# Optimization experiments

Hardware: AMD Instinct MI355X
Metric: run time of the kernel (lower is better)

The kernel has to match this reference:

```python
import jax, jax.numpy as jnp
import numpy as np
from jax import lax

# Dimensions
B, CIN, COUT = 8, 3, 3
NF = 128          # num_features
K = 9             # DISCO kernel_shape (number of filter basis functions)
HLAT, WLON = 181, 360   # in_shape == out_shape (1-degree equiangular sphere grid)
KH, KW = 5, 5     # compact lat/lon support of each DISCO basis function


def setup_inputs() -> dict:
    key = jax.random.key(0)
    ks = jax.random.split(key, 10)
    s = lambda fan: 1.0 / np.sqrt(fan)
    return {
        "x": jax.random.normal(ks[0], (B, CIN, HLAT, WLON), jnp.float32),
        # DISCO conv: latitude-dependent basis filters, quadrature weights, channel mix
        "psi": jax.random.normal(ks[1], (K, HLAT, KH, KW), jnp.float32) * s(KH * KW),
        "quad": jnp.abs(jax.random.normal(ks[2], (HLAT,), jnp.float32)) * (1.0 / HLAT)
                + jnp.sin(jnp.pi * (jnp.arange(HLAT) + 0.5) / HLAT) * (1.0 / HLAT),
        "w1": jax.random.normal(ks[3], (NF, CIN, K), jnp.float32) * s(CIN * K),
        "b1": jnp.zeros((NF,), jnp.float32),
        # standard conv2d stages
        "w2": jax.random.normal(ks[4], (NF // 2, NF, 5, 5), jnp.float32) * s(NF * 25),
        "b2": jnp.zeros((NF // 2,), jnp.float32),
        "w3": jax.random.normal(ks[5], (COUT, NF // 2, 5, 5), jnp.float32) * s(NF // 2 * 25),
        "b3": jnp.zeros((COUT,), jnp.float32),
    }


def _disco_conv_s2(x, psi, quad, w, b):
    """Discrete-continuous spherical conv: latitude-dependent gather + weighted sum.
    x: [B,C,H,W]; psi: [K,H,KH,KW]; quad: [H]; w: [O,C,K]; b: [O] -> [B,O,H,W]"""
    H, W = x.shape[-2], x.shape[-1]
    rh, rw = KH // 2, KW // 2
    xw = x * quad[None, None, :, None]                       # quadrature-weighted input
    # neighborhood indices: clipped in latitude, circular in longitude
    hi = jnp.clip(jnp.arange(H)[:, None] + jnp.arange(KH)[None, :] - rh, 0, H - 1)  # [H,KH]
    wi = (jnp.arange(W)[:, None] + jnp.arange(KW)[None, :] - rw) % W                # [W,KW]
    g = xw[:, :, hi, :]                                      # [B,C,H,KH,W]
    patches = g[:, :, :, :, wi]                              # [B,C,H,KH,W,KW]
    # project onto latitude-dependent filter basis, then mix channels per basis
    z = jnp.einsum('khij,bchiwj->bckhw', psi, patches)       # [B,C,K,H,W]
    return jnp.einsum('ock,bckhw->bohw', w, z) + b[None, :, None, None]


def _conv2d(x, w, b, pad):
    y = lax.conv_general_dilated(x, w, (1, 1), [(pad, pad), (pad, pad)],
                                 dimension_numbers=('NCHW', 'OIHW', 'NCHW'))
    return y + b[None, :, None, None]


def reference(x, psi, quad, w1, b1, w2, b2, w3, b3):
    h = jax.nn.relu(_disco_conv_s2(x, psi, quad, w1, b1))
    h = jax.nn.relu(_conv2d(h, w2, b2, 2))
    return _conv2d(h, w3, b3, 2)
```

## Files before the change

### kernel.cpp

```cpp
#include <hip/hip_runtime.h>
#include <hip/hip_bf16.h>

#define HLAT 181
#define WLON 360
#define HW (HLAT * WLON)
#define HPAD 188
#define WPAD 368
#define PCHH ((size_t)HPAD * WPAD * 8)
#define W2P 372
#define PLANE2 ((size_t)HPAD * W2P * 64)
#define ZROW ((size_t)12 * 4 * 32 * 16)

typedef __attribute__((ext_vector_type(4)))  short short4v;
typedef __attribute__((ext_vector_type(8)))  short short8v;
typedef __attribute__((ext_vector_type(4)))  float f32x4;
typedef __attribute__((ext_vector_type(16))) float f32x16;

static __device__ __forceinline__ ushort bf16_hi_bits(float f) {
  union { float f; unsigned u; } c; c.f = f;
  unsigned u = c.u;
  unsigned rounded = u + 0x7FFF + ((u >> 16) & 1);
  return (ushort)(rounded >> 16);
}
static __device__ __forceinline__ float bf16_to_f(ushort b) {
  union { unsigned u; float f; } c; c.u = ((unsigned)b) << 16;
  return c.f;
}

__global__ __launch_bounds__(256) void k_tw(const float* __restrict__ w2,
                                            const float* __restrict__ w3,
                                            const float* __restrict__ w1,
                                            const float* __restrict__ b1,
                                            ushort* __restrict__ w2f,
                                            ushort* __restrict__ w1f,
                                            ushort* __restrict__ w3f) {
  int idx = blockIdx.x * 256 + threadIdx.x;
  if (idx < 51200) {
    int l   = idx & 63;
    int p   = (idx >> 6) & 1;
    int m   = (idx >> 7) & 1;
    int ch  = (idx >> 8) & 7;
    int tap = idx >> 11;
    int oc  = m * 32 + (l & 31);
    int ci0 = ch * 16 + (l >> 5) * 8;
#pragma unroll
    for (int j = 0; j < 8; ++j) {
      float f = w2[(oc * 128 + ci0 + j) * 25 + tap];
      ushort hi = bf16_hi_bits(f);
      w2f[(size_t)idx * 8 + j] = (p == 0) ? hi : bf16_hi_bits(f - bf16_to_f(hi));
    }
  }
  if (idx < 1024) {
    int l = idx & 63;
    int e = idx >> 6;
    int p  = e & 1;
    int kc = (e >> 1) & 1;
    int m  = e >> 2;
    int oc = m * 32 + (l & 31);
    int k0 = kc * 16 + (l >> 5) * 8;
#pragma unroll
    for (int j = 0; j < 8; ++j) {
      int k = k0 + j;
      float f = (k < 27) ? w1[oc * 27 + k] : (k == 27 ? b1[oc] : 0.f);
      ushort hi = bf16_hi_bits(f);
      w1f[(size_t)idx * 8 + j] = (p == 0) ? hi : bf16_hi_bits(f - bf16_to_f(hi));
    }
  }
  if (idx < 6400) {
    int l   = idx & 63;
    int p   = (idx >> 6) & 1;
    int kc  = (idx >> 7) & 1;
    int tap = idx >> 8;
    int oc  = l & 15;
    int ci0 = kc * 32 + (l >> 4) * 8;
#pragma unroll
    for (int j = 0; j < 8; ++j) {
      float f = (oc < 3) ? w3[(oc * 64 + ci0 + j) * 25 + tap] : 0.f;
      ushort hi = bf16_hi_bits(f);
      w3f[(size_t)idx * 8 + j] = (p == 0) ? hi : bf16_hi_bits(f - bf16_to_f(hi));
    }
  }
}

__global__ __launch_bounds__(256) void k_zring(ushort* __restrict__ h1s) {
  const int i = blockIdx.x * 256 + threadIdx.x;
  if (i >= 4024) return;
  int row, col;
  if (i < 736)       { row = i / 368;              col = i % 368; }
  else if (i < 2576) { int p = i - 736;  row = 183 + p / 368; col = p % 368; }
  else if (i < 2938) { int p = i - 2576; row = 2 + p % 181;   col = p / 181; }
  else               { int p = i - 2938; row = 2 + p % 181;   col = 362 + p / 181; }
  short8v z = {0, 0, 0, 0, 0, 0, 0, 0};
  *(short8v*)(h1s + (size_t)blockIdx.y * PCHH + ((size_t)row * 368 + col) * 8) = z;
}

__global__ __launch_bounds__(256) void k_zring2(ushort* __restrict__ h2p) {
  const int i = blockIdx.x * 256 + threadIdx.x;
  if (i >= 4776) return;
  int row, col;
  if (i < 744)       { row = i / W2P;             col = i % W2P; }
  else if (i < 2604) { int p = i - 744;  row = 183 + p / W2P; col = p % W2P; }
  else               { int p = i - 2604; row = 2 + p % 181;
                       int cI = p / 181; col = (cI < 2) ? cI : 360 + cI; }
  short8v z = {0, 0, 0, 0, 0, 0, 0, 0};
  short8v* d = (short8v*)(h2p + (size_t)blockIdx.y * PLANE2 + ((size_t)row * W2P + col) * 64);
#pragma unroll
  for (int k = 0; k < 8; ++k) d[k] = z;
}

__global__ __launch_bounds__(384, 2) void k_z(const float* __restrict__ x,
    const float* __restrict__ psi, const float* __restrict__ quad,
    ushort* __restrict__ zbuf, int b0) {
  const int h = blockIdx.x;
  const int bi = blockIdx.y;
  const int b = b0 + bi;
  const int tid = threadIdx.x;
  float z[28];
#pragma unroll
  for (int q = 0; q < 28; ++q) z[q] = 0.f;
  if (tid < 360) {
#pragma unroll 1
    for (int i = 0; i < 5; ++i) {
      int hi = h + i - 2;
      hi = hi < 0 ? 0 : (hi >= HLAT ? HLAT - 1 : hi);
      const float qv = quad[hi];
      float pv[45];
#pragma unroll
      for (int kk = 0; kk < 9; ++kk)
#pragma unroll
        for (int j = 0; j < 5; ++j)
          pv[kk * 5 + j] = psi[((size_t)(kk * HLAT + h)) * 25 + i * 5 + j];
#pragma unroll
      for (int c = 0; c < 3; ++c) {
        const float* row = x + ((size_t)(b * 3 + c) * HLAT + hi) * WLON;
        float v[5];
#pragma unroll
        for (int j = 0; j < 5; ++j) {
          int wj = tid + j - 2;
          wj = wj < 0 ? wj + WLON : (wj >= WLON ? wj - WLON : wj);
          v[j] = row[wj] * qv;
        }
#pragma unroll
        for (int kk = 0; kk < 9; ++kk) {
          float a = 0.f;
#pragma unroll
          for (int j = 0; j < 5; ++j) a += pv[kk * 5 + j] * v[j];
          z[c * 9 + kk] += a;
        }
      }
    }
    z[27] = 1.0f;
  }
  ushort hiv[32], lov[32];
#pragma unroll
  for (int q = 0; q < 28; ++q) {
    const ushort hb = bf16_hi_bits(z[q]);
    hiv[q] = hb;
    lov[q] = bf16_hi_bits(z[q] - bf16_to_f(hb));
  }
#pragma unroll
  for (int q = 28; q < 32; ++q) { hiv[q] = 0; lov[q] = 0; }

  ushort* tb = zbuf + (size_t)(bi * HLAT + h) * ZROW +
               (size_t)(tid >> 5) * 2048 + (size_t)(tid & 31) * 16;
#pragma unroll
  for (int pk = 0; pk < 4; ++pk) {
    const ushort* src = (pk < 2 ? hiv : lov) + (pk & 1) * 16;
    union { ushort u[8]; short8v v8; } a0, a1;
#pragma unroll
    for (int j = 0; j < 8; ++j) { a0.u[j] = src[j]; a1.u[j] = src[8 + j]; }
    *(short8v*)(tb + (size_t)pk * 512 + 0) = a0.v8;
    *(short8v*)(tb + (size_t)pk * 512 + 8) = a1.v8;
  }
}

__global__ __launch_bounds__(256, 2) void k_mv(const ushort* __restrict__ zbuf,
    const ushort* __restrict__ w1f, ushort* __restrict__ h1s) {
  __shared__ ushort st[4][16][32][16];
  const int h = blockIdx.x;
  const int bi = blockIdx.y;
  const int tid = threadIdx.x;
  const int wv = tid >> 6;
  const int l = tid & 63;
  const int l31 = l & 31;
  const int q = l >> 5;
  const short8v* wf1 = (const short8v*)w1f;
  short8v A[4][2][2];
#pragma unroll
  for (int m = 0; m < 4; ++m)
#pragma unroll
    for (int kc = 0; kc < 2; ++kc)
#pragma unroll
      for (int p = 0; p < 2; ++p)
        A[m][kc][p] = wf1[(size_t)(((m * 2 + kc) * 2 + p) * 64 + l)];

  ushort* base = h1s + (size_t)bi * 32 * PCHH;
  const ushort* zrow = zbuf + (size_t)(bi * HLAT + h) * ZROW;
#pragma unroll
  for (int nn = 0; nn < 3; ++nn) {
    const int n = wv * 3 + nn;
    const ushort* zn = zrow + (size_t)n * 2048 + l31 * 16 + q * 8;
    const short8v bh0 = *(const short8v*)(zn + 0);
    const short8v bh1 = *(const short8v*)(zn + 512);
    const short8v bl0 = *(const short8v*)(zn + 1024);
    const short8v bl1 = *(const short8v*)(zn + 1536);
#pragma unroll
    for (int m = 0; m < 4; ++m) {
      f32x16 acc;
#pragma unroll
      for (int e = 0; e < 16; ++e) acc[e] = 0.f;
      acc = __builtin_amdgcn_mfma_f32_32x32x16_bf16(A[m][0][0], bh0, acc, 0, 0, 0);
      acc = __builtin_amdgcn_mfma_f32_32x32x16_bf16(A[m][0][1], bh0, acc, 0, 0, 0);
      acc = __builtin_amdgcn_mfma_f32_32x32x16_bf16(A[m][0][0], bl0, acc, 0, 0, 0);
      acc = __builtin_amdgcn_mfma_f32_32x32x16_bf16(A[m][1][0], bh1, acc, 0, 0, 0);
      acc = __builtin_amdgcn_mfma_f32_32x32x16_bf16(A[m][1][1], bh1, acc, 0, 0, 0);
      acc = __builtin_amdgcn_mfma_f32_32x32x16_bf16(A[m][1][0], bl1, acc, 0, 0, 0);
#pragma unroll
      for (int r = 0; r < 4; ++r) {
        const int rb = 8 * r + 4 * q;
        const int p2h = m * 2 + (rb >> 4);
        const int ci0 = rb & 15;
        short4v h4, l4;
#pragma unroll
        for (int j = 0; j < 4; ++j) {
          const float v = fmaxf(acc[r * 4 + j], 0.f);
          const ushort hb = bf16_hi_bits(v);
          h4[j] = (short)hb;
          l4[j] = (short)bf16_hi_bits(v - bf16_to_f(hb));
        }
        *(short4v*)&st[wv][p2h][l31][ci0] = h4;
        *(short4v*)&st[wv][8 + p2h][l31][ci0] = l4;
      }
    }
    const int pxr = n * 32 + (l >> 1);
    if (pxr < 360) {
      const size_t po = ((size_t)(h + 2) * WPAD + (pxr + 2)) * 8;
#pragma unroll
      for (int p2 = 0; p2 < 16; ++p2) {
        const short8v v = *(const short8v*)&st[wv][p2][l >> 1][(l & 1) * 8];
        *(short8v*)(base + (size_t)(p2 * 2 + (l & 1)) * PCHH + po) = v;
      }
    }
  }
}

__global__ __launch_bounds__(256, 2) void k_conv2(const ushort* __restrict__ h1s,
    const ushort* __restrict__ w2f, const float* __restrict__ b2,
    ushort* __restrict__ h2p) {
  __shared__ ushort act[2][15360];
  const int x0 = blockIdx.x * 32;
  const int y0 = blockIdx.y * 8;
  const int bi = blockIdx.z;
  const int tid = threadIdx.x;
  const int wv = tid >> 6;
  const int m  = wv >> 1;
  const int wr = wv & 1;
  const int l = tid & 63;
  const int l31 = l & 31;
  const int q = l >> 5;

  f32x16 acc[4];
#pragma unroll
  for (int r = 0; r < 4; ++r)
#pragma unroll
    for (int e = 0; e < 16; ++e) acc[r][e] = 0.f;

  const short8v* wf = (const short8v*)w2f;
  const ushort* pbase = h1s + (size_t)bi * 32 * PCHH;

  unsigned goff[8];
#pragma unroll
  for (int s = 0; s < 8; ++s) {
    const int idx = (wv * 8 + s) * 64 + l;
    const int reg = idx / 480;
    const int rem = idx - reg * 480;
    const int t = rem / 40;
    const int c = rem - t * 40;
    const int part = reg >> 1, qq = reg & 1;
    goff[s] = (unsigned)((part * 16 + qq) * PCHH) +
              (unsigned)(((y0 + t) * WPAD + (x0 + c)) * 8);
  }

  auto stage = [&](int buf, int ch) {
    const size_t choff = (size_t)ch * 2 * PCHH;
#pragma unroll
    for (int s = 0; s < 8; ++s) {
      if (wv * 8 + s < 30) {
        const ushort* g = pbase + choff + goff[s];
        ushort* d = &act[buf][(wv * 8 + s) * 512];
        __builtin_amdgcn_global_load_lds(
            (const __attribute__((address_space(1))) unsigned int*)g,
            (__attribute__((address_space(3))) unsigned int*)d, 16, 0, 0);
      }
    }
  };

  stage(0, 0);
  asm volatile("s_waitcnt vmcnt(0)" ::: "memory");
  __syncthreads();

#pragma unroll 1
  for (int ch = 0; ch < 8; ++ch) {
    const int cur = ch & 1;
    if (ch < 7) stage(cur ^ 1, ch + 1);
#pragma unroll 1
    for (int dj = 0; dj < 5; ++dj) {
      short8v aw[5][2];
#pragma unroll
      for (int di = 0; di < 5; ++di) {
        const size_t e0 = (size_t)(((di * 5 + dj) * 8 + ch) * 4 + m * 2) * 64 + l;
        aw[di][0] = wf[e0];
        aw[di][1] = wf[e0 + 64];
      }
      const unsigned rbase = q * 3840 + (l31 + dj) * 8;
      __builtin_amdgcn_s_setprio(1);
#pragma unroll
      for (int rr = 0; rr < 8; ++rr) {
        const int t = wr * 4 + rr;
        const short8v bh = *(const short8v*)&act[cur][rbase + t * 320];
        const short8v bl = *(const short8v*)&act[cur][7680 + rbase + t * 320];
#pragma unroll
        for (int di = 0; di < 5; ++di) {
          const int r = rr - di;
          if (r < 0 || r > 3) continue;
          acc[r] = __builtin_amdgcn_mfma_f32_32x32x16_bf16(aw[di][0], bh, acc[r], 0, 0, 0);
          acc[r] = __builtin_amdgcn_mfma_f32_32x32x16_bf16(aw[di][1], bh, acc[r], 0, 0, 0);
          acc[r] = __builtin_amdgcn_mfma_f32_32x32x16_bf16(aw[di][0], bl, acc[r], 0, 0, 0);
        }
      }
      __builtin_amdgcn_s_setprio(0);
    }
    asm volatile("s_waitcnt vmcnt(0)" ::: "memory");
    __syncthreads();
  }

  const int xg = x0 + l31;
  ushort* hp = h2p + (size_t)bi * 2 * PLANE2;
  if (xg < WLON) {
#pragma unroll
    for (int r = 0; r < 4; ++r) {
      const int y = y0 + wr * 4 + r;
      if (y >= HLAT) continue;
      const size_t po = ((size_t)(y + 2) * W2P + (xg + 2)) * 64;
#pragma unroll
      for (int run = 0; run < 4; ++run) {
        const int oc0 = m * 32 + 8 * run + 4 * q;
        short4v h4, l4;
#pragma unroll
        for (int j = 0; j < 4; ++j) {
          const float v = fmaxf(acc[r][run * 4 + j] + b2[oc0 + j], 0.f);
          const ushort hb = bf16_hi_bits(v);
          h4[j] = (short)hb;
          l4[j] = (short)bf16_hi_bits(v - bf16_to_f(hb));
        }
        *(short4v*)(hp + po + oc0) = h4;
        *(short4v*)(hp + PLANE2 + po + oc0) = l4;
      }
    }
  }
}

__global__ __launch_bounds__(256, 2) void k_conv3(const ushort* __restrict__ h2p,
    const ushort* __restrict__ w3f, const float* __restrict__ b3,
    float* __restrict__ out, int b0) {
  __shared__ ushort act[2][12][20][72];
  const int x0 = blockIdx.x * 16;
  const int y0 = blockIdx.y * 8;
  const int bi = blockIdx.z;
  const int tid = threadIdx.x;
  const int wv = tid >> 6;
  const int l = tid & 63;

  {
    const ushort* pb = h2p + (size_t)bi * 2 * PLANE2;
    float4 v[6][3];
#pragma unroll
    for (int pr = 0; pr < 6; ++pr) {
      const int pair = wv * 6 + pr;
      const int part = pair / 12;
      const int row = pair % 12;
      const ushort* src = pb + (size_t)part * PLANE2 +
                          ((size_t)(y0 + row) * W2P + x0) * 64;
      v[pr][0] = *(const float4*)((const char*)src + l * 16);
      v[pr][1] = *(const float4*)((const char*)src + 1024 + l * 16);
      if (l < 32) v[pr][2] = *(const float4*)((const char*)src + 2048 + l * 16);
    }
#pragma unroll
    for (int pr = 0; pr < 6; ++pr) {
      const int pair = wv * 6 + pr;
      const int part = pair / 12;
      const int row = pair % 12;
#pragma unroll
      for (int k2 = 0; k2 < 3; ++k2) {
        if (k2 == 2 && l >= 32) continue;
        const int B = k2 * 1024 + l * 16;
        const int col = B >> 7;
        const int ci = (B & 127) >> 1;
        *(short8v*)&act[part][row][col][ci] = *(short8v*)&v[pr][k2];
      }
    }
  }
  __syncthreads();

  f32x4 acc[2];
#pragma unroll
  for (int r = 0; r < 2; ++r)
#pragma unroll
    for (int e = 0; e < 4; ++e) acc[r][e] = 0.f;

  const short8v* wf3 = (const short8v*)w3f;
  const int c16 = l & 15;
  const int koff0 = ((l >> 4) & 3) * 8;

#pragma unroll 1
  for (int kc = 0; kc < 2; ++kc) {
#pragma unroll 1
    for (int dj = 0; dj < 5; ++dj) {
      short8v A[5][2];
#pragma unroll
      for (int di = 0; di < 5; ++di) {
        const size_t e0 = (size_t)(((di * 5 + dj) * 2 + kc) * 2) * 64 + l;
        A[di][0] = wf3[e0];
        A[di][1] = wf3[e0 + 64];
      }
      const int c = c16 + dj;
      const int koff = kc * 32 + koff0;
      __builtin_amdgcn_s_setprio(1);
#pragma unroll
      for (int tt = 0; tt < 6; ++tt) {
        const int t = wv * 2 + tt;
        const short8v bh = *(const short8v*)&act[0][t][c][koff];
        const short8v bl = *(const short8v*)&act[1][t][c][koff];
#pragma unroll
        for (int di = 0; di < 5; ++di) {
          const int r = tt - di;
          if (r < 0 || r > 1) continue;
          acc[r] = __builtin_amdgcn_mfma_f32_16x16x32_bf16(A[di][0], bh, acc[r], 0, 0, 0);
          acc[r] = __builtin_amdgcn_mfma_f32_16x16x32_bf16(A[di][1], bh, acc[r], 0, 0, 0);
          acc[r] = __builtin_amdgcn_mfma_f32_16x16x32_bf16(A[di][0], bl, acc[r], 0, 0, 0);
        }
      }
      __builtin_amdgcn_s_setprio(0);
    }
  }

  const int px = x0 + c16;
  const int b = b0 + bi;
  if ((l >> 4) == 0 && px < WLON) {
    const float bb[3] = {b3[0], b3[1], b3[2]};
#pragma unroll
    for (int r = 0; r < 2; ++r) {
      const int y = y0 + wv * 2 + r;
      if (y >= HLAT) continue;
#pragma unroll
      for (int j = 0; j < 3; ++j)
        out[((size_t)(b * 3 + j) * HLAT + y) * WLON + px] = acc[r][j] + bb[j];
    }
  }
}

extern "C" void kernel_launch(void* const* d_in, const int* in_sizes, int n_in,
                              void* d_out, int out_size, void* d_ws, size_t ws_size,
                              hipStream_t stream) {
  const float* x    = (const float*)d_in[0];
  const float* psi  = (const float*)d_in[1];
  const float* quad = (const float*)d_in[2];
  const float* w1   = (const float*)d_in[3];
  const float* b1   = (const float*)d_in[4];
  const float* w2   = (const float*)d_in[5];
  const float* b2   = (const float*)d_in[6];
  const float* w3   = (const float*)d_in[7];
  const float* b3   = (const float*)d_in[8];
  float* out = (float*)d_out;
  float* ws  = (float*)d_ws;

  ushort* w2f = (ushort*)ws;
  ushort* w1f = (ushort*)(ws + 204800);
  ushort* w3f = (ushort*)(ws + 208896);
  const size_t HEAD = 234496;

  size_t wsf = ws_size / 4;
  const size_t h1s_f = PCHH * 16;
  const size_t h2p_f = PLANE2;
  const size_t per_b = h1s_f + h2p_f;
  int bc = 8;
  while (bc > 1 && HEAD + (size_t)bc * per_b > wsf) bc >>= 1;

  ushort* h1s = (ushort*)(ws + HEAD);
  ushort* h2p = (ushort*)(ws + HEAD + (size_t)bc * h1s_f);
  ushort* zbuf = h2p;

  k_tw<<<dim3(200), dim3(256), 0, stream>>>(w2, w3, w1, b1, w2f, w1f, w3f);
  k_zring<<<dim3(16, bc * 32), dim3(256), 0, stream>>>(h1s);

  for (int b0 = 0; b0 < 8; b0 += bc) {
    int cur = 8 - b0 < bc ? 8 - b0 : bc;
    k_z<<<dim3(HLAT, cur), dim3(384), 0, stream>>>(x, psi, quad, zbuf, b0);
    k_mv<<<dim3(HLAT, cur), dim3(256), 0, stream>>>(zbuf, w1f, h1s);
    k_zring2<<<dim3(19, cur * 2), dim3(256), 0, stream>>>(h2p);
    k_conv2<<<dim3(12, 23, cur), dim3(256), 0, stream>>>(h1s, w2f, b2, h2p);
    k_conv3<<<dim3(23, 23, cur), dim3(256), 0, stream>>>(h2p, w3f, b3, out, b0);
  }
}
```

Before: 763.1 us.

## Split conv2 into 8-wave blocks staging hi and lo activation parts separately

Doubles the conv2 block from 4 to 8 waves, with each wave computing 2 output rows instead of 4. This halves the accumulator registers and raises the occupancy target. Activation staging is split into separate hi and lo bf16 parts held in two half-size LDS buffers. The hi part runs the two weight-split MFMAs and the lo part runs one MFMA. This halves shared memory per block and frees registers, but it adds a barrier per part and exposes load latency, since the next channel's hi part is loaded only after the lo buffer is ready. Each wave also reloads the weight fragments for every row group.

After: 878.7 us. 1.15x slower.

```diff
diff --git a/kernel.cpp b/kernel.cpp
--- a/kernel.cpp
+++ b/kernel.cpp
@@ -244,50 +244,49 @@
   }
 }
 
-__global__ __launch_bounds__(256, 2) void k_conv2(const ushort* __restrict__ h1s,
+__global__ __launch_bounds__(512, 4) void k_conv2(const ushort* __restrict__ h1s,
     const ushort* __restrict__ w2f, const float* __restrict__ b2,
     ushort* __restrict__ h2p) {
-  __shared__ ushort act[2][15360];
+  __shared__ ushort act[2][7680];
   const int x0 = blockIdx.x * 32;
   const int y0 = blockIdx.y * 8;
   const int bi = blockIdx.z;
   const int tid = threadIdx.x;
   const int wv = tid >> 6;
-  const int m  = wv >> 1;
-  const int wr = wv & 1;
+  const int m  = wv >> 2;
+  const int wr = wv & 3;
   const int l = tid & 63;
   const int l31 = l & 31;
   const int q = l >> 5;
 
-  f32x16 acc[4];
-#pragma unroll
-  for (int r = 0; r < 4; ++r)
+  f32x16 acc[2];
+#pragma unroll
+  for (int r = 0; r < 2; ++r)
 #pragma unroll
     for (int e = 0; e < 16; ++e) acc[r][e] = 0.f;
 
   const short8v* wf = (const short8v*)w2f;
   const ushort* pbase = h1s + (size_t)bi * 32 * PCHH;
 
-  unsigned goff[8];
-#pragma unroll
-  for (int s = 0; s < 8; ++s) {
-    const int idx = (wv * 8 + s) * 64 + l;
-    const int reg = idx / 480;
-    const int rem = idx - reg * 480;
+  unsigned goff[2];
+#pragma unroll
+  for (int s = 0; s < 2; ++s) {
+    const int gi = (wv * 2 + s) * 64 + l;
+    const int qq = gi / 480;
+    const int rem = gi - qq * 480;
     const int t = rem / 40;
     const int c = rem - t * 40;
-    const int part = reg >> 1, qq = reg & 1;
-    goff[s] = (unsigned)((part * 16 + qq) * PCHH) +
+    goff[s] = (unsigned)(qq * PCHH) +
               (unsigned)(((y0 + t) * WPAD + (x0 + c)) * 8);
   }
 
-  auto stage = [&](int buf, int ch) {
-    const size_t choff = (size_t)ch * 2 * PCHH;
-#pragma unroll
-    for (int s = 0; s < 8; ++s) {
-      if (wv * 8 + s < 30) {
-        const ushort* g = pbase + choff + goff[s];
-        ushort* d = &act[buf][(wv * 8 + s) * 512];
+  auto stage = [&](int buf, int ch, int part) {
+    const size_t poff = (size_t)(part * 16 + ch * 2) * PCHH;
+#pragma unroll
+    for (int s = 0; s < 2; ++s) {
+      if (wv * 2 + s < 15) {
+        const ushort* g = pbase + poff + goff[s];
+        ushort* d = &act[buf][(wv * 2 + s) * 512];
         __builtin_amdgcn_global_load_lds(
             (const __attribute__((address_space(1))) unsigned int*)g,
             (__attribute__((address_space(3))) unsigned int*)d, 16, 0, 0);
@@ -295,15 +294,14 @@
     }
   };
 
-  stage(0, 0);
+  stage(0, 0, 0);
   asm volatile("s_waitcnt vmcnt(0)" ::: "memory");
   __syncthreads();
 
 #pragma unroll 1
   for (int ch = 0; ch < 8; ++ch) {
-    const int cur = ch & 1;
-    if (ch < 7) stage(cur ^ 1, ch + 1);
-#pragma unroll 1
+    stage(1, ch, 1);
+#pragma unroll
     for (int dj = 0; dj < 5; ++dj) {
       short8v aw[5][2];
 #pragma unroll
@@ -315,17 +313,41 @@
       const unsigned rbase = q * 3840 + (l31 + dj) * 8;
       __builtin_amdgcn_s_setprio(1);
 #pragma unroll
-      for (int rr = 0; rr < 8; ++rr) {
-        const int t = wr * 4 + rr;
-        const short8v bh = *(const short8v*)&act[cur][rbase + t * 320];
-        const short8v bl = *(const short8v*)&act[cur][7680 + rbase + t * 320];
+      for (int rr = 0; rr < 6; ++rr) {
+        const int t = wr * 2 + rr;
+        const short8v bh = *(const short8v*)&act[0][rbase + t * 320];
 #pragma unroll
         for (int di = 0; di < 5; ++di) {
           const int r = rr - di;
-          if (r < 0 || r > 3) continue;
+          if (r < 0 || r > 1) continue;
           acc[r] = __builtin_amdgcn_mfma_f32_32x32x16_bf16(aw[di][0], bh, acc[r], 0, 0, 0);
           acc[r] = __builtin_amdgcn_mfma_f32_32x32x16_bf16(aw[di][1], bh, acc[r], 0, 0, 0);
-          acc[r] = __builtin_amdgcn_mfma_f32_32x32x16_bf16(aw[di][0], bl, acc[r], 0, 0, 0);
+        }
+      }
+      __builtin_amdgcn_s_setprio(0);
+    }
+    asm volatile("s_waitcnt vmcnt(0)" ::: "memory");
+    __syncthreads();
+    if (ch < 7) stage(0, ch + 1, 0);
+#pragma unroll
+    for (int dj = 0; dj < 5; ++dj) {
+      short8v awh[5];
+#pragma unroll
+      for (int di = 0; di < 5; ++di) {
+        const size_t e0 = (size_t)(((di * 5 + dj) * 8 + ch) * 4 + m * 2) * 64 + l;
+        awh[di] = wf[e0];
+      }
+      const unsigned rbase = q * 3840 + (l31 + dj) * 8;
+      __builtin_amdgcn_s_setprio(1);
+#pragma unroll
+      for (int rr = 0; rr < 6; ++rr) {
+        const int t = wr * 2 + rr;
+        const short8v bl = *(const short8v*)&act[1][rbase + t * 320];
+#pragma unroll
+        for (int di = 0; di < 5; ++di) {
+          const int r = rr - di;
+          if (r < 0 || r > 1) continue;
+          acc[r] = __builtin_amdgcn_mfma_f32_32x32x16_bf16(awh[di], bl, acc[r], 0, 0, 0);
         }
       }
       __builtin_amdgcn_s_setprio(0);
@@ -338,8 +360,8 @@
   ushort* hp = h2p + (size_t)bi * 2 * PLANE2;
   if (xg < WLON) {
 #pragma unroll
-    for (int r = 0; r < 4; ++r) {
-      const int y = y0 + wr * 4 + r;
+    for (int r = 0; r < 2; ++r) {
+      const int y = y0 + wr * 2 + r;
       if (y >= HLAT) continue;
       const size_t po = ((size_t)(y + 2) * W2P + (xg + 2)) * 64;
 #pragma unroll
@@ -498,7 +520,7 @@
     k_z<<<dim3(HLAT, cur), dim3(384), 0, stream>>>(x, psi, quad, zbuf, b0);
     k_mv<<<dim3(HLAT, cur), dim3(256), 0, stream>>>(zbuf, w1f, h1s);
     k_zring2<<<dim3(19, cur * 2), dim3(256), 0, stream>>>(h2p);
-    k_conv2<<<dim3(12, 23, cur), dim3(256), 0, stream>>>(h1s, w2f, b2, h2p);
+    k_conv2<<<dim3(12, 23, cur), dim3(512), 0, stream>>>(h1s, w2f, b2, h2p);
     k_conv3<<<dim3(23, 23, cur), dim3(256), 0, stream>>>(h2p, w3f, b3, out, b0);
   }
 }
```
